# Kernel optimization log

Hardware: AMD Instinct MI355X
Metric: run time of the kernel (lower is better)

## Reference

```python
import jax, jax.numpy as jnp
import numpy as np

EPS = 1e-12
B, DIN, T, DH = 32, 512, 4096, 500


def setup_inputs() -> dict:
    key = jax.random.key(0)
    k1, k2, k3 = jax.random.split(key, 3)
    x = jax.random.normal(k1, (B, DIN, T), dtype=jnp.float32)
    weight1 = jax.random.normal(k2, (DH, DIN), dtype=jnp.float32) * (1.0 / np.sqrt(DIN))
    weight2 = jax.random.normal(k3, (1, DH), dtype=jnp.float32) * (1.0 / np.sqrt(DH))
    return {"x": x, "weight1": weight1, "weight2": weight2, "dim": 2}


def reference(x, weight1, weight2, dim):
    # x: (B, din, T)
    h = jnp.swapaxes(x, 1, 2)                      # (B, T, din)
    a = jax.nn.relu(jnp.einsum('btd,hd->bth', h, weight1))  # (B, T, dh)
    scores = jnp.einsum('bth,oh->bto', a, weight2)           # (B, T, 1)
    attn = jax.nn.softmax(scores, axis=1)                    # softmax over time
    mean = jnp.einsum('bdt,bto->bdo', x, attn)               # (B, din, 1)
    variance = jnp.mean((x - mean) ** 2, axis=dim)           # (B, din) unweighted
    mean_s = jnp.squeeze(mean, axis=dim)                     # (B, din)
    mask = (variance <= EPS).astype(variance.dtype)
    variance = (1.0 - mask) * variance + mask * EPS
    stddev = jnp.sqrt(variance)
    return jnp.concatenate((mean_s, stddev), axis=-1)        # (B, 2*din)
```

## Files before the change

### kernel.cpp

```cpp
#include <hip/hip_runtime.h>
#include <hip/hip_bf16.h>

#define NB 32
#define DIN 512
#define TT 4096
#define DH 500
#define DHP 512
#define EPSV 1e-12f
#define BM 64
#define LDA 520
#define NTILES (TT / BM)
#define CH 8
#define NCH 4

typedef short short8 __attribute__((ext_vector_type(8)));
typedef float f32x16 __attribute__((ext_vector_type(16)));

__device__ inline unsigned short f2bf(float f) {
    unsigned int u = __builtin_bit_cast(unsigned int, f);
    unsigned int r = (u + 0x7fffu + ((u >> 16) & 1u)) >> 16;
    return (unsigned short)r;
}
__device__ inline float bf2f(unsigned short h) {
    unsigned int u = ((unsigned int)h) << 16;
    return __builtin_bit_cast(float, u);
}

__global__ void prep_kernel(const float* __restrict__ w1, const float* __restrict__ w2,
                            unsigned short* __restrict__ w1b, float* __restrict__ w2f) {
    int idx = blockIdx.x * blockDim.x + threadIdx.x;
    if (idx < DHP * DIN) {
        const int j    = idx & 7;
        const int lane = (idx >> 3) & 63;
        const int ks   = (idx >> 9) & 31;
        const int hb   = idx >> 14;
        const int h = hb * 32 + (lane & 31);
        const int d = ks * 16 + (lane >> 5) * 8 + j;
        float v = (h < DH) ? w1[h * DIN + d] : 0.f;
        w1b[idx] = f2bf(v);
        if (idx < DHP) w2f[idx] = (idx < DH) ? w2[idx] : 0.f;
    }
}

__launch_bounds__(512, 2)
__global__ void scores_fused(const float* __restrict__ x,
                             const unsigned short* __restrict__ w1b,
                             const float* __restrict__ w2f,
                             float* __restrict__ pm, float* __restrict__ pz,
                             float* __restrict__ pswx, float* __restrict__ psx,
                             float* __restrict__ psx2) {
    __shared__ unsigned short A_lds[BM][LDA];
    __shared__ float score_p[8][BM];
    __shared__ float w_lds[BM];

    const int tid = threadIdx.x;
    const int b = blockIdx.x >> 6;
    const int t0 = (blockIdx.x & 63) * BM;

    {
        const int ts = tid & 63;
        const int dg = tid >> 6;
        const float* xb = x + (size_t)b * DIN * TT + t0 + ts;
        #pragma unroll
        for (int oct = 0; oct < 8; ++oct) {
            const int d0 = dg * 64 + oct * 8;
            short8 pk;
            #pragma unroll
            for (int j = 0; j < 8; ++j)
                pk[j] = (short)f2bf(xb[(size_t)(d0 + j) * TT]);
            *reinterpret_cast<short8*>(&A_lds[ts][d0]) = pk;
        }
    }
    __syncthreads();

    const int w = tid >> 6;
    const int lane = tid & 63;
    const int lane31 = lane & 31;
    const int khalf = lane >> 5;
    const int hrow0 = w * 64;

    float w20v[16], w21v[16];
    #pragma unroll
    for (int g = 0; g < 16; ++g) {
        const int rp = (g & 3) + 8 * (g >> 2) + 4 * khalf;
        w20v[g] = w2f[hrow0 + rp];
        w21v[g] = w2f[hrow0 + 32 + rp];
    }

    f32x16 acc00, acc01, acc10, acc11;
    #pragma unroll
    for (int g = 0; g < 16; ++g) { acc00[g] = 0.f; acc01[g] = 0.f; acc10[g] = 0.f; acc11[g] = 0.f; }

    const unsigned short* base0 = w1b + (size_t)w * 32768 + (size_t)lane * 8;
    const unsigned short* base1 = base0 + 16384;
    const unsigned short* Bp0 = &A_lds[lane31][khalf * 8];
    const unsigned short* Bp1 = &A_lds[32 + lane31][khalf * 8];

    short8 a0buf[2][CH], a1buf[2][CH];
    #pragma unroll
    for (int j = 0; j < CH; ++j) {
        a0buf[0][j] = *reinterpret_cast<const short8*>(base0 + j * 512);
        a1buf[0][j] = *reinterpret_cast<const short8*>(base1 + j * 512);
    }
    #pragma unroll
    for (int c = 0; c < NCH; ++c) {
        if (c + 1 < NCH) {
            #pragma unroll
            for (int j = 0; j < CH; ++j) {
                a0buf[(c + 1) & 1][j] = *reinterpret_cast<const short8*>(base0 + ((c + 1) * CH + j) * 512);
                a1buf[(c + 1) & 1][j] = *reinterpret_cast<const short8*>(base1 + ((c + 1) * CH + j) * 512);
            }
        }
        __builtin_amdgcn_sched_barrier(0);
        #pragma unroll
        for (int j = 0; j < CH; ++j) {
            const int ks = c * CH + j;
            short8 b0 = *reinterpret_cast<const short8*>(Bp0 + ks * 16);
            short8 b1 = *reinterpret_cast<const short8*>(Bp1 + ks * 16);
            acc00 = __builtin_amdgcn_mfma_f32_32x32x16_bf16(a0buf[c & 1][j], b0, acc00, 0, 0, 0);
            acc01 = __builtin_amdgcn_mfma_f32_32x32x16_bf16(a0buf[c & 1][j], b1, acc01, 0, 0, 0);
            acc10 = __builtin_amdgcn_mfma_f32_32x32x16_bf16(a1buf[c & 1][j], b0, acc10, 0, 0, 0);
            acc11 = __builtin_amdgcn_mfma_f32_32x32x16_bf16(a1buf[c & 1][j], b1, acc11, 0, 0, 0);
        }
        __builtin_amdgcn_sched_barrier(0);
    }

    float s0 = 0.f, s1 = 0.f;
    #pragma unroll
    for (int g = 0; g < 16; ++g) {
        s0 += fmaxf(acc00[g], 0.f) * w20v[g] + fmaxf(acc10[g], 0.f) * w21v[g];
        s1 += fmaxf(acc01[g], 0.f) * w20v[g] + fmaxf(acc11[g], 0.f) * w21v[g];
    }
    s0 += __shfl_xor(s0, 32, 64);
    s1 += __shfl_xor(s1, 32, 64);
    if (khalf == 0) {
        score_p[w][lane31] = s0;
        score_p[w][32 + lane31] = s1;
    }
    __syncthreads();

    if (tid < BM) {
        float s = 0.f;
        #pragma unroll
        for (int ww = 0; ww < 8; ++ww) s += score_p[ww][tid];
        float m = s;
        #pragma unroll
        for (int k = 1; k <= 32; k <<= 1) m = fmaxf(m, __shfl_xor(m, k, 64));
        float e = __expf(s - m);
        float Z = e;
        #pragma unroll
        for (int k = 1; k <= 32; k <<= 1) Z += __shfl_xor(Z, k, 64);
        w_lds[tid] = e;
        if (tid == 0) { pm[blockIdx.x] = m; pz[blockIdx.x] = Z; }
    }
    __syncthreads();

    {
        const int d = tid;
        float sx = 0.f, sx2 = 0.f, swx = 0.f;
        #pragma unroll 8
        for (int t = 0; t < BM; ++t) {
            const float xv = bf2f(A_lds[t][d]);
            const float wv = w_lds[t];
            sx += xv; sx2 += xv * xv; swx += wv * xv;
        }
        const size_t o = (size_t)blockIdx.x * DHP + d;
        psx[o] = sx; psx2[o] = sx2; pswx[o] = swx;
    }
}

__global__ void combine_kernel(const float* __restrict__ pm, const float* __restrict__ pz,
                               const float* __restrict__ pswx, const float* __restrict__ psx,
                               const float* __restrict__ psx2, float* __restrict__ out) {
    __shared__ float sm[NTILES], sz[NTILES];
    const int b = blockIdx.x;
    const int tid = threadIdx.x;
    if (tid < NTILES) { sm[tid] = pm[b * NTILES + tid]; sz[tid] = pz[b * NTILES + tid]; }
    __syncthreads();

    float mg = -1e30f;
    #pragma unroll 8
    for (int i = 0; i < NTILES; ++i) mg = fmaxf(mg, sm[i]);
    float denom = 0.f;
    #pragma unroll 8
    for (int i = 0; i < NTILES; ++i) denom += sz[i] * __expf(sm[i] - mg);

    float num = 0.f, sx = 0.f, sx2 = 0.f;
    #pragma unroll 4
    for (int i = 0; i < NTILES; ++i) {
        const size_t o = ((size_t)(b * NTILES + i)) * DHP + tid;
        const float f = __expf(sm[i] - mg);
        num += f * pswx[o];
        sx  += psx[o];
        sx2 += psx2[o];
    }
    const float mean = num / denom;
    const float ex  = sx  * (1.f / TT);
    const float ex2 = sx2 * (1.f / TT);
    float var = ex2 - 2.f * mean * ex + mean * mean;
    if (var <= EPSV) var = EPSV;
    out[(size_t)b * 1024 + tid] = mean;
    out[(size_t)b * 1024 + 512 + tid] = sqrtf(var);
}

extern "C" void kernel_launch(void* const* d_in, const int* in_sizes, int n_in,
                              void* d_out, int out_size, void* d_ws, size_t ws_size,
                              hipStream_t stream) {
    const float* x  = (const float*)d_in[0];
    const float* w1 = (const float*)d_in[1];
    const float* w2 = (const float*)d_in[2];
    float* out = (float*)d_out;

    char* ws = (char*)d_ws;
    unsigned short* w1b = (unsigned short*)ws;
    float* w2f  = (float*)(ws + 524288);
    float* pm   = (float*)(ws + 526336);
    float* pz   = (float*)(ws + 534528);
    float* pswx = (float*)(ws + 542720);
    float* psx  = pswx + (size_t)NB * NTILES * DHP;
    float* psx2 = psx  + (size_t)NB * NTILES * DHP;

    prep_kernel<<<(DHP * DIN + 255) / 256, 256, 0, stream>>>(w1, w2, w1b, w2f);
    scores_fused<<<NB * NTILES, 512, 0, stream>>>(x, w1b, w2f, pm, pz, pswx, psx, psx2);
    combine_kernel<<<NB, 512, 0, stream>>>(pm, pz, pswx, psx, psx2, out);
}
```

Baseline: 141.6 us.

## Double time tile, overlap x loads with MFMA over K chunks, drop weight prefetch

Each block now handles 128 time steps instead of 64, so every W1 fragment loaded from global memory feeds four MFMA tiles and the weight traffic per time step is halved. The x tile is loaded in four K chunks: the next chunk's global loads are issued before the MFMA work on the current chunk and converted into LDS afterward, overlapping global latency with compute. The register double-buffered W1 prefetch is removed and the softmax reduction now spans two wavefronts through a small shared array. In exchange the kernel uses more accumulator registers and LDS, adds one barrier per chunk, and launches half as many blocks, which may lower occupancy.

Result: faster. 129.2 us (-8.8%).

```diff
diff --git a/kernel.cpp b/kernel.cpp
--- a/kernel.cpp
+++ b/kernel.cpp
@@ -7,11 +7,11 @@
 #define DH 500
 #define DHP 512
 #define EPSV 1e-12f
-#define BM 64
+#define BM 128
 #define LDA 520
 #define NTILES (TT / BM)
-#define CH 8
-#define NCH 4
+#define CHD 128
+#define NCHK 4
 
 typedef short short8 __attribute__((ext_vector_type(8)));
 typedef float f32x16 __attribute__((ext_vector_type(16)));
@@ -52,108 +52,123 @@
     __shared__ unsigned short A_lds[BM][LDA];
     __shared__ float score_p[8][BM];
     __shared__ float w_lds[BM];
+    __shared__ float red[4];
 
     const int tid = threadIdx.x;
-    const int b = blockIdx.x >> 6;
-    const int t0 = (blockIdx.x & 63) * BM;
-
-    {
-        const int ts = tid & 63;
-        const int dg = tid >> 6;
-        const float* xb = x + (size_t)b * DIN * TT + t0 + ts;
-        #pragma unroll
-        for (int oct = 0; oct < 8; ++oct) {
-            const int d0 = dg * 64 + oct * 8;
-            short8 pk;
-            #pragma unroll
-            for (int j = 0; j < 8; ++j)
-                pk[j] = (short)f2bf(xb[(size_t)(d0 + j) * TT]);
-            *reinterpret_cast<short8*>(&A_lds[ts][d0]) = pk;
-        }
-    }
-    __syncthreads();
+    const int b  = blockIdx.x >> 5;
+    const int t0 = (blockIdx.x & 31) * BM;
+
+    const int tsub  = tid & 63;
+    const int thalf = (tid >> 6) & 1;
+    const int ts    = thalf * 64 + tsub;
+    const int dg    = tid >> 7;
+    const float* xb = x + (size_t)b * DIN * TT + t0 + ts;
 
     const int w = tid >> 6;
     const int lane = tid & 63;
     const int lane31 = lane & 31;
     const int khalf = lane >> 5;
     const int hrow0 = w * 64;
-
-    float w20v[16], w21v[16];
-    #pragma unroll
-    for (int g = 0; g < 16; ++g) {
-        const int rp = (g & 3) + 8 * (g >> 2) + 4 * khalf;
-        w20v[g] = w2f[hrow0 + rp];
-        w21v[g] = w2f[hrow0 + 32 + rp];
-    }
-
-    f32x16 acc00, acc01, acc10, acc11;
-    #pragma unroll
-    for (int g = 0; g < 16; ++g) { acc00[g] = 0.f; acc01[g] = 0.f; acc10[g] = 0.f; acc11[g] = 0.f; }
-
     const unsigned short* base0 = w1b + (size_t)w * 32768 + (size_t)lane * 8;
     const unsigned short* base1 = base0 + 16384;
-    const unsigned short* Bp0 = &A_lds[lane31][khalf * 8];
-    const unsigned short* Bp1 = &A_lds[32 + lane31][khalf * 8];
-
-    short8 a0buf[2][CH], a1buf[2][CH];
-    #pragma unroll
-    for (int j = 0; j < CH; ++j) {
-        a0buf[0][j] = *reinterpret_cast<const short8*>(base0 + j * 512);
-        a1buf[0][j] = *reinterpret_cast<const short8*>(base1 + j * 512);
-    }
-    #pragma unroll
-    for (int c = 0; c < NCH; ++c) {
-        if (c + 1 < NCH) {
-            #pragma unroll
-            for (int j = 0; j < CH; ++j) {
-                a0buf[(c + 1) & 1][j] = *reinterpret_cast<const short8*>(base0 + ((c + 1) * CH + j) * 512);
-                a1buf[(c + 1) & 1][j] = *reinterpret_cast<const short8*>(base1 + ((c + 1) * CH + j) * 512);
+
+    {
+        float xr[32];
+        #pragma unroll
+        for (int j = 0; j < 32; ++j)
+            xr[j] = xb[(size_t)(dg * 32 + j) * TT];
+        #pragma unroll
+        for (int oct = 0; oct < 4; ++oct) {
+            short8 pk;
+            #pragma unroll
+            for (int j = 0; j < 8; ++j) pk[j] = (short)f2bf(xr[oct * 8 + j]);
+            *reinterpret_cast<short8*>(&A_lds[ts][dg * 32 + oct * 8]) = pk;
+        }
+    }
+    __syncthreads();
+
+    f32x16 acc[2][4];
+    #pragma unroll
+    for (int p = 0; p < 2; ++p)
+        #pragma unroll
+        for (int tt = 0; tt < 4; ++tt)
+            #pragma unroll
+            for (int g = 0; g < 16; ++g) acc[p][tt][g] = 0.f;
+
+    #pragma unroll
+    for (int c = 0; c < NCHK; ++c) {
+        float xr[32];
+        if (c < NCHK - 1) {
+            const int db = (c + 1) * CHD + dg * 32;
+            #pragma unroll
+            for (int j = 0; j < 32; ++j)
+                xr[j] = xb[(size_t)(db + j) * TT];
+        }
+        __builtin_amdgcn_sched_barrier(0);
+
+        #pragma unroll
+        for (int ks = 0; ks < 8; ++ks) {
+            const int k = c * 8 + ks;
+            short8 a0 = *reinterpret_cast<const short8*>(base0 + k * 512);
+            short8 a1 = *reinterpret_cast<const short8*>(base1 + k * 512);
+            #pragma unroll
+            for (int tt = 0; tt < 4; ++tt) {
+                short8 bb = *reinterpret_cast<const short8*>(
+                    &A_lds[tt * 32 + lane31][k * 16 + khalf * 8]);
+                acc[0][tt] = __builtin_amdgcn_mfma_f32_32x32x16_bf16(a0, bb, acc[0][tt], 0, 0, 0);
+                acc[1][tt] = __builtin_amdgcn_mfma_f32_32x32x16_bf16(a1, bb, acc[1][tt], 0, 0, 0);
             }
         }
-        __builtin_amdgcn_sched_barrier(0);
-        #pragma unroll
-        for (int j = 0; j < CH; ++j) {
-            const int ks = c * CH + j;
-            short8 b0 = *reinterpret_cast<const short8*>(Bp0 + ks * 16);
-            short8 b1 = *reinterpret_cast<const short8*>(Bp1 + ks * 16);
-            acc00 = __builtin_amdgcn_mfma_f32_32x32x16_bf16(a0buf[c & 1][j], b0, acc00, 0, 0, 0);
-            acc01 = __builtin_amdgcn_mfma_f32_32x32x16_bf16(a0buf[c & 1][j], b1, acc01, 0, 0, 0);
-            acc10 = __builtin_amdgcn_mfma_f32_32x32x16_bf16(a1buf[c & 1][j], b0, acc10, 0, 0, 0);
-            acc11 = __builtin_amdgcn_mfma_f32_32x32x16_bf16(a1buf[c & 1][j], b1, acc11, 0, 0, 0);
-        }
-        __builtin_amdgcn_sched_barrier(0);
-    }
-
-    float s0 = 0.f, s1 = 0.f;
-    #pragma unroll
-    for (int g = 0; g < 16; ++g) {
-        s0 += fmaxf(acc00[g], 0.f) * w20v[g] + fmaxf(acc10[g], 0.f) * w21v[g];
-        s1 += fmaxf(acc01[g], 0.f) * w20v[g] + fmaxf(acc11[g], 0.f) * w21v[g];
-    }
-    s0 += __shfl_xor(s0, 32, 64);
-    s1 += __shfl_xor(s1, 32, 64);
-    if (khalf == 0) {
-        score_p[w][lane31] = s0;
-        score_p[w][32 + lane31] = s1;
-    }
-    __syncthreads();
-
+
+        if (c < NCHK - 1) {
+            const int db = (c + 1) * CHD + dg * 32;
+            #pragma unroll
+            for (int oct = 0; oct < 4; ++oct) {
+                short8 pk;
+                #pragma unroll
+                for (int j = 0; j < 8; ++j) pk[j] = (short)f2bf(xr[oct * 8 + j]);
+                *reinterpret_cast<short8*>(&A_lds[ts][db + oct * 8]) = pk;
+            }
+        }
+        __syncthreads();
+    }
+
+    #pragma unroll
+    for (int tt = 0; tt < 4; ++tt) {
+        float s = 0.f;
+        #pragma unroll
+        for (int g = 0; g < 16; ++g) {
+            const int rp = (g & 3) + 8 * (g >> 2) + 4 * khalf;
+            s += fmaxf(acc[0][tt][g], 0.f) * w2f[hrow0 + rp]
+               + fmaxf(acc[1][tt][g], 0.f) * w2f[hrow0 + 32 + rp];
+        }
+        s += __shfl_xor(s, 32, 64);
+        if (khalf == 0) score_p[w][tt * 32 + lane31] = s;
+    }
+    __syncthreads();
+
+    const int tl = tid & 127;
+    float sv = 0.f;
     if (tid < BM) {
-        float s = 0.f;
-        #pragma unroll
-        for (int ww = 0; ww < 8; ++ww) s += score_p[ww][tid];
-        float m = s;
-        #pragma unroll
-        for (int k = 1; k <= 32; k <<= 1) m = fmaxf(m, __shfl_xor(m, k, 64));
-        float e = __expf(s - m);
-        float Z = e;
-        #pragma unroll
-        for (int k = 1; k <= 32; k <<= 1) Z += __shfl_xor(Z, k, 64);
-        w_lds[tid] = e;
-        if (tid == 0) { pm[blockIdx.x] = m; pz[blockIdx.x] = Z; }
-    }
-    __syncthreads();
+        #pragma unroll
+        for (int ww = 0; ww < 8; ++ww) sv += score_p[ww][tl];
+    }
+    float m = (tid < BM) ? sv : -1e30f;
+    #pragma unroll
+    for (int k = 1; k <= 32; k <<= 1) m = fmaxf(m, __shfl_xor(m, k, 64));
+    if (tid == 0) red[0] = m;
+    if (tid == 64) red[1] = m;
+    __syncthreads();
+    const float mb = fmaxf(red[0], red[1]);
+    float e = 0.f, Zp = 0.f;
+    if (tid < BM) { e = __expf(sv - mb); Zp = e; }
+    #pragma unroll
+    for (int k = 1; k <= 32; k <<= 1) Zp += __shfl_xor(Zp, k, 64);
+    if (tid == 0) red[2] = Zp;
+    if (tid == 64) red[3] = Zp;
+    if (tid < BM) w_lds[tl] = e;
+    __syncthreads();
+    if (tid == 0) { pm[blockIdx.x] = mb; pz[blockIdx.x] = red[2] + red[3]; }
 
     {
         const int d = tid;
@@ -215,8 +230,8 @@
     unsigned short* w1b = (unsigned short*)ws;
     float* w2f  = (float*)(ws + 524288);
     float* pm   = (float*)(ws + 526336);
-    float* pz   = (float*)(ws + 534528);
-    float* pswx = (float*)(ws + 542720);
+    float* pz   = (float*)(ws + 530432);
+    float* pswx = (float*)(ws + 534528);
     float* psx  = pswx + (size_t)NB * NTILES * DHP;
     float* psx2 = psx  + (size_t)NB * NTILES * DHP;
 
```
